# Performance work log

Measured on AMD Instinct MI355X. Metric: run time of the kernel, lower is better.

The kernel has to match this reference:

```python
import jax, jax.numpy as jnp
import numpy as np

N = 50000      # n_nodes
E = 800000     # n_edges
IN_CH = 128
HID = 128
OUT_CH = 64
N_LAYERS = 4


def _linear_params(key, fan_in, fan_out):
    kw, kb = jax.random.split(key)
    bound = 1.0 / np.sqrt(fan_in)
    W = jax.random.uniform(kw, (fan_out, fan_in), jnp.float32, -bound, bound)
    b = jax.random.uniform(kb, (fan_out,), jnp.float32, -bound, bound)
    return W, b


def setup_inputs() -> dict:
    key = jax.random.key(0)
    ks = jax.random.split(key, 5)
    x = jax.random.normal(ks[0], (N, IN_CH), jnp.float32)
    edge_index = jax.random.randint(ks[1], (2, E), 0, N, dtype=jnp.int64)
    W_in, b_in = _linear_params(ks[2], IN_CH, HID)
    conv_keys = jax.random.split(ks[3], N_LAYERS)
    Wc = jnp.stack([_linear_params(k, HID, HID)[0] for k in conv_keys])
    bc = jnp.stack([_linear_params(k, HID, HID)[1] for k in conv_keys])
    W_out, b_out = _linear_params(ks[4], HID * N_LAYERS, OUT_CH)
    return {"x": x, "edge_index": edge_index, "W_in": W_in, "b_in": b_in,
            "Wc": Wc, "bc": bc, "W_out": W_out, "b_out": b_out}


def reference(x, edge_index, W_in, b_in, Wc, bc, W_out, b_out):
    n = x.shape[0]
    # input projection + relu
    x = jax.nn.relu(x @ W_in.T + b_in)
    src, dst = edge_index[0], edge_index[1]
    loop = jnp.arange(n, dtype=edge_index.dtype)
    src_a = jnp.concatenate([src, loop])   # [E+N]
    dst_a = jnp.concatenate([dst, loop])   # [E+N]
    # symmetric-normalized degree (with self loops)
    deg = jax.ops.segment_sum(jnp.ones(src_a.shape[0], x.dtype), dst_a, num_segments=n)
    norm = (deg[src_a] * deg[dst_a]) ** -0.5
    norm = jnp.where(jnp.isinf(norm), 0.0, norm)  # guard deg==0 (original sets inf->0)
    layer_outputs = []
    for i in range(Wc.shape[0]):
        h = x @ Wc[i].T + bc[i]                     # [N, HID]
        msg = h[src_a] * norm[:, None]              # gather + scale  [E+N, HID]
        out = jax.ops.segment_sum(msg, dst_a, num_segments=n)  # scatter-add
        x = jax.nn.relu(out)
        layer_outputs.append(x)
    h = jnp.concatenate(layer_outputs, axis=-1)     # jk_mode='cat' -> [N, HID*L]
    return h @ W_out.T + b_out
```

## Files before the change

kernel.cpp:

```cpp
#include <hip/hip_runtime.h>
#include <hip/hip_bf16.h>

#ifndef MIN
#define MIN(a,b) ((a)<(b)?(a):(b))
#endif

typedef _Float16 half2_t __attribute__((ext_vector_type(2)));
typedef _Float16 half4_t __attribute__((ext_vector_type(4)));
typedef _Float16 half8_t __attribute__((ext_vector_type(8)));
typedef float floatx4 __attribute__((ext_vector_type(4)));

#define BUCKET_SHIFT 6
#define BUCKET_SIZE 64
#define SCHUNK 2048


__global__ void hist_kernel(const int* __restrict__ dst, int E,
                            int* __restrict__ bucketCnt, int NB) {
    __shared__ int h[1024];
    int t = threadIdx.x;
    for (int i = t; i < 1024; i += 256) h[i] = 0;
    __syncthreads();
    for (int e = blockIdx.x * 256 + t; e < E; e += gridDim.x * 256)
        atomicAdd(&h[dst[e] >> BUCKET_SHIFT], 1);
    __syncthreads();
    for (int i = t; i < NB; i += 256)
        if (h[i]) atomicAdd(&bucketCnt[i], h[i]);
}

__global__ void bucket_scan(const int* __restrict__ bucketCnt,
                            int* __restrict__ bucketBase, int* __restrict__ bucketCur,
                            int NB, int E) {
    __shared__ int sm[1024];
    int t = threadIdx.x;
    int v = (t < NB) ? bucketCnt[t] : 0;
    sm[t] = v;
    __syncthreads();
    for (int off = 1; off < 1024; off <<= 1) {
        int add = (t >= off) ? sm[t - off] : 0;
        __syncthreads();
        sm[t] += add;
        __syncthreads();
    }
    if (t < NB) {
        bucketBase[t] = sm[t] - v;
        bucketCur[t] = sm[t] - v;
    }
    if (t == 0) bucketBase[NB] = E;
}

__global__ void scatter_kernel(const int* __restrict__ src, const int* __restrict__ dst,
                               int E, int* __restrict__ bucketCur,
                               unsigned int* __restrict__ rec) {
    __shared__ int hist[1024];
    __shared__ int base[1024];
    int t = threadIdx.x;
    int e0 = blockIdx.x * SCHUNK;
    int e1 = MIN(E, e0 + SCHUNK);
    for (int i = t; i < 1024; i += 256) hist[i] = 0;
    __syncthreads();
    for (int e = e0 + t; e < e1; e += 256)
        atomicAdd(&hist[dst[e] >> BUCKET_SHIFT], 1);
    __syncthreads();
    for (int i = t; i < 1024; i += 256) {
        int c = hist[i];
        base[i] = c ? atomicAdd(&bucketCur[i], c) : 0;
        hist[i] = 0;
    }
    __syncthreads();
    for (int e = e0 + t; e < e1; e += 256) {
        int d = dst[e];
        int b = d >> BUCKET_SHIFT;
        int pos = base[b] + atomicAdd(&hist[b], 1);
        rec[pos] = (unsigned)src[e] | ((unsigned)(d & (BUCKET_SIZE - 1)) << 16);
    }
}

__global__ void bucket_build(const unsigned int* __restrict__ rec,
                             const int* __restrict__ bucketBase,
                             int* __restrict__ rowptr, unsigned short* __restrict__ csr_src,
                             float* __restrict__ dinv, int N, int E) {
    __shared__ int lcnt[256];
    __shared__ int sm[256];
    __shared__ int lcur[64];
    int b = blockIdx.x;
    int t = threadIdx.x;
    int beg = bucketBase[b], end = bucketBase[b + 1];
    lcnt[t] = 0;
    __syncthreads();
    for (int i = beg + t; i < end; i += 256)
        atomicAdd(&lcnt[rec[i] >> 16], 1);
    __syncthreads();
    int v = lcnt[t];
    sm[t] = v;
    __syncthreads();
    for (int off = 1; off < 256; off <<= 1) {
        int add = (t >= off) ? sm[t - off] : 0;
        __syncthreads();
        sm[t] += add;
        __syncthreads();
    }
    int excl = sm[t] - v;
    if (t < BUCKET_SIZE) {
        int node = b * BUCKET_SIZE + t;
        if (node < N) {
            rowptr[node] = beg + excl;
            dinv[node] = rsqrtf((float)(v + 1));
        }
        lcur[t] = beg + excl;
    }
    __syncthreads();
    for (int i = beg + t; i < end; i += 256) {
        unsigned int r = rec[i];
        int pos = atomicAdd(&lcur[r >> 16], 1);
        csr_src[pos] = (unsigned short)(r & 0xFFFFu);
    }
    if (b == 0 && t == 0) rowptr[N] = E;
}


__global__ void cvt_weights(const float* __restrict__ a, _Float16* __restrict__ oa, int na,
                            const float* __restrict__ b, _Float16* __restrict__ ob, int nb,
                            const float* __restrict__ c, _Float16* __restrict__ oc, int nc) {
    int i = blockIdx.x * blockDim.x + threadIdx.x;
    if (i < na) oa[i] = (_Float16)a[i];
    if (i < nb) ob[i] = (_Float16)b[i];
    if (i < nc) oc[i] = (_Float16)c[i];
}


__global__ void agg_kernel(const half2_t* __restrict__ Hb, const float* __restrict__ dinv,
                           const int* __restrict__ rowptr,
                           const unsigned short* __restrict__ csr_src,
                           half2_t* __restrict__ X, int N) {
    int node = blockIdx.x * 4 + (threadIdx.x >> 6);
    int t = threadIdx.x & 63;
    if (node >= N) return;
    float di = dinv[node];
    half2_t hu = Hb[(size_t)node * 64 + t];
    float2 acc;
    acc.x = (float)hu.x * di;
    acc.y = (float)hu.y * di;
    int beg = rowptr[node];
    int end = rowptr[node + 1];

    for (int base = beg; base < end; base += 64) {
        int idx = base + t;
        bool valid = idx < end;
        int s_lane = valid ? (int)csr_src[idx] : node;
        float w_lane = valid ? dinv[s_lane] : 0.0f;
        int m = end - base;
        if (m > 64) m = 64;
        int mm = (m + 7) & ~7;
        for (int j = 0; j < mm; j += 8) {
            int s0 = __shfl(s_lane, j + 0), s1 = __shfl(s_lane, j + 1);
            int s2 = __shfl(s_lane, j + 2), s3 = __shfl(s_lane, j + 3);
            int s4 = __shfl(s_lane, j + 4), s5 = __shfl(s_lane, j + 5);
            int s6 = __shfl(s_lane, j + 6), s7 = __shfl(s_lane, j + 7);
            float w0 = __shfl(w_lane, j + 0), w1 = __shfl(w_lane, j + 1);
            float w2 = __shfl(w_lane, j + 2), w3 = __shfl(w_lane, j + 3);
            float w4 = __shfl(w_lane, j + 4), w5 = __shfl(w_lane, j + 5);
            float w6 = __shfl(w_lane, j + 6), w7 = __shfl(w_lane, j + 7);
            half2_t u0 = Hb[(size_t)s0 * 64 + t];
            half2_t u1 = Hb[(size_t)s1 * 64 + t];
            half2_t u2 = Hb[(size_t)s2 * 64 + t];
            half2_t u3 = Hb[(size_t)s3 * 64 + t];
            half2_t u4 = Hb[(size_t)s4 * 64 + t];
            half2_t u5 = Hb[(size_t)s5 * 64 + t];
            half2_t u6 = Hb[(size_t)s6 * 64 + t];
            half2_t u7 = Hb[(size_t)s7 * 64 + t];
            acc.x = fmaf((float)u0.x, w0, acc.x); acc.y = fmaf((float)u0.y, w0, acc.y);
            acc.x = fmaf((float)u1.x, w1, acc.x); acc.y = fmaf((float)u1.y, w1, acc.y);
            acc.x = fmaf((float)u2.x, w2, acc.x); acc.y = fmaf((float)u2.y, w2, acc.y);
            acc.x = fmaf((float)u3.x, w3, acc.x); acc.y = fmaf((float)u3.y, w3, acc.y);
            acc.x = fmaf((float)u4.x, w4, acc.x); acc.y = fmaf((float)u4.y, w4, acc.y);
            acc.x = fmaf((float)u5.x, w5, acc.x); acc.y = fmaf((float)u5.y, w5, acc.y);
            acc.x = fmaf((float)u6.x, w6, acc.x); acc.y = fmaf((float)u6.y, w6, acc.y);
            acc.x = fmaf((float)u7.x, w7, acc.x); acc.y = fmaf((float)u7.y, w7, acc.y);
        }
    }
    half2_t o;
    o.x = (_Float16)fmaxf(acc.x * di, 0.0f);
    o.y = (_Float16)fmaxf(acc.y * di, 0.0f);
    X[(size_t)node * 256 + t] = o;
}


template <int BN, int KCH, bool A_F16, bool RELU, bool BIAS, bool F16OUT>
__global__ __launch_bounds__(256)
void mfma_gemm(const void* __restrict__ Av, int lda,
               const _Float16* __restrict__ W, int ldw,
               const float* __restrict__ bias,
               void* __restrict__ Cv, int ldc, int M) {
    constexpr int NT = BN / 16;
    __shared__ __align__(16) _Float16 Ws[BN][136];

    int tid = threadIdx.x;
    int rowBase = blockIdx.x * 64;
    int w = tid >> 6;
    int lane = tid & 63;
    int lrow = lane & 15;
    int quad = lane >> 4;
    int kq = quad * 8;
    int gr = rowBase + w * 16 + lrow;

    floatx4 acc[NT];
#pragma unroll
    for (int nt = 0; nt < NT; ++nt) acc[nt] = (floatx4){0.f, 0.f, 0.f, 0.f};

#pragma unroll
    for (int kc = 0; kc < KCH; ++kc) {
#pragma unroll
        for (int i = tid; i < BN * 16; i += 256) {
            int n = i >> 4, k8 = (i & 15) * 8;
            uint4 v = *(const uint4*)(W + (size_t)n * ldw + kc * 128 + k8);
            *(uint4*)(&Ws[n][k8]) = v;
        }
        __syncthreads();

        half8_t a[4];
        if (gr < M) {
            if (A_F16) {
                const _Float16* A = (const _Float16*)Av;
                const _Float16* ap = A + (size_t)gr * lda + kc * 128 + kq;
#pragma unroll
                for (int ks = 0; ks < 4; ++ks)
                    a[ks] = *(const half8_t*)(ap + ks * 32);
            } else {
                const float* A = (const float*)Av;
                const float* ap = A + (size_t)gr * lda + kc * 128 + kq;
#pragma unroll
                for (int ks = 0; ks < 4; ++ks) {
                    float4 v0 = *(const float4*)(ap + ks * 32);
                    float4 v1 = *(const float4*)(ap + ks * 32 + 4);
                    half8_t h;
                    h[0] = (_Float16)v0.x; h[1] = (_Float16)v0.y;
                    h[2] = (_Float16)v0.z; h[3] = (_Float16)v0.w;
                    h[4] = (_Float16)v1.x; h[5] = (_Float16)v1.y;
                    h[6] = (_Float16)v1.z; h[7] = (_Float16)v1.w;
                    a[ks] = h;
                }
            }
        } else {
#pragma unroll
            for (int ks = 0; ks < 4; ++ks)
                a[ks] = (half8_t){0, 0, 0, 0, 0, 0, 0, 0};
        }

#pragma unroll
        for (int ks = 0; ks < 4; ++ks) {
            int kk = ks * 32 + kq;
#pragma unroll
            for (int nt = 0; nt < NT; ++nt) {
                half8_t b = *(const half8_t*)(&Ws[nt * 16 + lrow][kk]);
                acc[nt] = __builtin_amdgcn_mfma_f32_16x16x32_f16(a[ks], b, acc[nt], 0, 0, 0);
            }
        }
        if (kc != KCH - 1) __syncthreads();
    }

#pragma unroll
    for (int nt = 0; nt < NT; ++nt) {
        int col = nt * 16 + lrow;
        float bv = BIAS ? bias[col] : 0.0f;
#pragma unroll
        for (int reg = 0; reg < 4; ++reg) {
            int gr2 = rowBase + w * 16 + quad * 4 + reg;
            if (gr2 < M) {
                float v = acc[nt][reg] + bv;
                if (RELU) v = fmaxf(v, 0.0f);
                if (F16OUT) {
                    _Float16* C = (_Float16*)Cv;
                    C[(size_t)gr2 * ldc + col] = (_Float16)v;
                } else {
                    float* C = (float*)Cv;
                    C[(size_t)gr2 * ldc + col] = v;
                }
            }
        }
    }
}


extern "C" void kernel_launch(void* const* d_in, const int* in_sizes, int n_in,
                              void* d_out, int out_size, void* d_ws, size_t ws_size,
                              hipStream_t stream) {
    const float* x     = (const float*)d_in[0];
    const int*   ei    = (const int*)d_in[1];
    const float* W_in  = (const float*)d_in[2];
    const float* b_in  = (const float*)d_in[3];
    const float* Wc    = (const float*)d_in[4];
    const float* bc    = (const float*)d_in[5];
    const float* W_out = (const float*)d_in[6];
    const float* b_out = (const float*)d_in[7];
    float* out = (float*)d_out;

    const int HID = 128;
    const int N = in_sizes[0] / HID;
    const int E = in_sizes[1] / 2;
    const int L = 4;
    const int* src = ei;
    const int* dst = ei + E;
    const int NB = (N + BUCKET_SIZE - 1) >> BUCKET_SHIFT;

    char* ws = (char*)d_ws;
    size_t off = 0;
    auto carve = [&](size_t bytes) {
        void* p = ws + off;
        off += (bytes + 255) & ~(size_t)255;
        return p;
    };
    float* dinv        = (float*)carve((size_t)N * 4);
    int*   rowptr      = (int*)carve((size_t)(N + 1) * 4);
    unsigned short* csr_src = (unsigned short*)carve((size_t)E * 2);
    unsigned int* rec  = (unsigned int*)carve((size_t)E * 4);
    int*   bucketCnt   = (int*)carve((size_t)1024 * 4);
    int*   bucketBase  = (int*)carve((size_t)1025 * 4);
    int*   bucketCur   = (int*)carve((size_t)1024 * 4);
    _Float16* bufA     = (_Float16*)carve((size_t)N * HID * 2);
    _Float16* bufH     = (_Float16*)carve((size_t)N * HID * 2);
    _Float16* bufXcat  = (_Float16*)carve((size_t)N * 512 * 2);
    _Float16* Wf_in    = (_Float16*)carve((size_t)HID * HID * 2);
    _Float16* Wf_c     = (_Float16*)carve((size_t)L * HID * HID * 2);
    _Float16* Wf_out   = (_Float16*)carve((size_t)64 * 512 * 2);
    (void)ws_size;

    hipMemsetAsync(bucketCnt, 0, (size_t)1024 * 4, stream);
    hist_kernel<<<512, 256, 0, stream>>>(dst, E, bucketCnt, NB);
    bucket_scan<<<1, 1024, 0, stream>>>(bucketCnt, bucketBase, bucketCur, NB, E);
    scatter_kernel<<<(E + SCHUNK - 1) / SCHUNK, 256, 0, stream>>>(src, dst, E, bucketCur, rec);
    bucket_build<<<NB, 256, 0, stream>>>(rec, bucketBase, rowptr, csr_src, dinv, N, E);

    cvt_weights<<<(L * HID * HID + 255) / 256, 256, 0, stream>>>(
        W_in, Wf_in, HID * HID,
        Wc, Wf_c, L * HID * HID,
        W_out, Wf_out, 64 * 512);

    int gemm_blocks = (N + 63) / 64;

    mfma_gemm<128, 1, false, true, true, true>
        <<<gemm_blocks, 256, 0, stream>>>(x, 128, Wf_in, HID, b_in, bufA, HID, N);

    for (int l = 0; l < L; ++l) {
        const void* Ain = (l == 0) ? (const void*)bufA
                                   : (const void*)(bufXcat + (size_t)(l - 1) * 128);
        int lda = (l == 0) ? 128 : 512;
        mfma_gemm<128, 1, true, false, true, true>
            <<<gemm_blocks, 256, 0, stream>>>(Ain, lda, Wf_c + (size_t)l * HID * HID, HID,
                                              bc + (size_t)l * HID, bufH, HID, N);
        agg_kernel<<<(N + 3) / 4, 256, 0, stream>>>((const half2_t*)bufH, dinv, rowptr,
                                                    csr_src,
                                                    (half2_t*)bufXcat + (size_t)l * 64, N);
    }

    mfma_gemm<64, 4, true, false, true, false>
        <<<gemm_blocks, 256, 0, stream>>>(bufXcat, 512, Wf_out, 512, b_out, out, 64, N);
}
```

Before: 326.3 us.

## Prescale GEMM output by dinv, fuse setup kernels, unweighted 16-wide aggregation

The layer GEMM epilogue now multiplies each row by its source-node dinv. The aggregation kernel can then sum neighbour rows without per-edge weight loads or shuffles, and it unrolls 16 gathers per step with padding pointing at a zeroed extra row. The histogram kernel is merged with the weight conversion, and the scatter kernel with the input projection GEMM, into single launches that split work by block index. This cuts per-edge dinv gathers, FMAs and launch count, at the cost of more wasted gathers on padded tails and larger kernels that may hold more registers.

```diff
diff --git a/kernel.cpp b/kernel.cpp
--- a/kernel.cpp
+++ b/kernel.cpp
@@ -15,188 +15,17 @@
 #define SCHUNK 2048
 
 
-__global__ void hist_kernel(const int* __restrict__ dst, int E,
-                            int* __restrict__ bucketCnt, int NB) {
-    __shared__ int h[1024];
-    int t = threadIdx.x;
-    for (int i = t; i < 1024; i += 256) h[i] = 0;
-    __syncthreads();
-    for (int e = blockIdx.x * 256 + t; e < E; e += gridDim.x * 256)
-        atomicAdd(&h[dst[e] >> BUCKET_SHIFT], 1);
-    __syncthreads();
-    for (int i = t; i < NB; i += 256)
-        if (h[i]) atomicAdd(&bucketCnt[i], h[i]);
-}
-
-__global__ void bucket_scan(const int* __restrict__ bucketCnt,
-                            int* __restrict__ bucketBase, int* __restrict__ bucketCur,
-                            int NB, int E) {
-    __shared__ int sm[1024];
-    int t = threadIdx.x;
-    int v = (t < NB) ? bucketCnt[t] : 0;
-    sm[t] = v;
-    __syncthreads();
-    for (int off = 1; off < 1024; off <<= 1) {
-        int add = (t >= off) ? sm[t - off] : 0;
-        __syncthreads();
-        sm[t] += add;
-        __syncthreads();
-    }
-    if (t < NB) {
-        bucketBase[t] = sm[t] - v;
-        bucketCur[t] = sm[t] - v;
-    }
-    if (t == 0) bucketBase[NB] = E;
-}
-
-__global__ void scatter_kernel(const int* __restrict__ src, const int* __restrict__ dst,
-                               int E, int* __restrict__ bucketCur,
-                               unsigned int* __restrict__ rec) {
-    __shared__ int hist[1024];
-    __shared__ int base[1024];
-    int t = threadIdx.x;
-    int e0 = blockIdx.x * SCHUNK;
-    int e1 = MIN(E, e0 + SCHUNK);
-    for (int i = t; i < 1024; i += 256) hist[i] = 0;
-    __syncthreads();
-    for (int e = e0 + t; e < e1; e += 256)
-        atomicAdd(&hist[dst[e] >> BUCKET_SHIFT], 1);
-    __syncthreads();
-    for (int i = t; i < 1024; i += 256) {
-        int c = hist[i];
-        base[i] = c ? atomicAdd(&bucketCur[i], c) : 0;
-        hist[i] = 0;
-    }
-    __syncthreads();
-    for (int e = e0 + t; e < e1; e += 256) {
-        int d = dst[e];
-        int b = d >> BUCKET_SHIFT;
-        int pos = base[b] + atomicAdd(&hist[b], 1);
-        rec[pos] = (unsigned)src[e] | ((unsigned)(d & (BUCKET_SIZE - 1)) << 16);
-    }
-}
-
-__global__ void bucket_build(const unsigned int* __restrict__ rec,
-                             const int* __restrict__ bucketBase,
-                             int* __restrict__ rowptr, unsigned short* __restrict__ csr_src,
-                             float* __restrict__ dinv, int N, int E) {
-    __shared__ int lcnt[256];
-    __shared__ int sm[256];
-    __shared__ int lcur[64];
-    int b = blockIdx.x;
-    int t = threadIdx.x;
-    int beg = bucketBase[b], end = bucketBase[b + 1];
-    lcnt[t] = 0;
-    __syncthreads();
-    for (int i = beg + t; i < end; i += 256)
-        atomicAdd(&lcnt[rec[i] >> 16], 1);
-    __syncthreads();
-    int v = lcnt[t];
-    sm[t] = v;
-    __syncthreads();
-    for (int off = 1; off < 256; off <<= 1) {
-        int add = (t >= off) ? sm[t - off] : 0;
-        __syncthreads();
-        sm[t] += add;
-        __syncthreads();
-    }
-    int excl = sm[t] - v;
-    if (t < BUCKET_SIZE) {
-        int node = b * BUCKET_SIZE + t;
-        if (node < N) {
-            rowptr[node] = beg + excl;
-            dinv[node] = rsqrtf((float)(v + 1));
-        }
-        lcur[t] = beg + excl;
-    }
-    __syncthreads();
-    for (int i = beg + t; i < end; i += 256) {
-        unsigned int r = rec[i];
-        int pos = atomicAdd(&lcur[r >> 16], 1);
-        csr_src[pos] = (unsigned short)(r & 0xFFFFu);
-    }
-    if (b == 0 && t == 0) rowptr[N] = E;
-}
-
-
-__global__ void cvt_weights(const float* __restrict__ a, _Float16* __restrict__ oa, int na,
-                            const float* __restrict__ b, _Float16* __restrict__ ob, int nb,
-                            const float* __restrict__ c, _Float16* __restrict__ oc, int nc) {
-    int i = blockIdx.x * blockDim.x + threadIdx.x;
-    if (i < na) oa[i] = (_Float16)a[i];
-    if (i < nb) ob[i] = (_Float16)b[i];
-    if (i < nc) oc[i] = (_Float16)c[i];
-}
-
-
-__global__ void agg_kernel(const half2_t* __restrict__ Hb, const float* __restrict__ dinv,
-                           const int* __restrict__ rowptr,
-                           const unsigned short* __restrict__ csr_src,
-                           half2_t* __restrict__ X, int N) {
-    int node = blockIdx.x * 4 + (threadIdx.x >> 6);
-    int t = threadIdx.x & 63;
-    if (node >= N) return;
-    float di = dinv[node];
-    half2_t hu = Hb[(size_t)node * 64 + t];
-    float2 acc;
-    acc.x = (float)hu.x * di;
-    acc.y = (float)hu.y * di;
-    int beg = rowptr[node];
-    int end = rowptr[node + 1];
-
-    for (int base = beg; base < end; base += 64) {
-        int idx = base + t;
-        bool valid = idx < end;
-        int s_lane = valid ? (int)csr_src[idx] : node;
-        float w_lane = valid ? dinv[s_lane] : 0.0f;
-        int m = end - base;
-        if (m > 64) m = 64;
-        int mm = (m + 7) & ~7;
-        for (int j = 0; j < mm; j += 8) {
-            int s0 = __shfl(s_lane, j + 0), s1 = __shfl(s_lane, j + 1);
-            int s2 = __shfl(s_lane, j + 2), s3 = __shfl(s_lane, j + 3);
-            int s4 = __shfl(s_lane, j + 4), s5 = __shfl(s_lane, j + 5);
-            int s6 = __shfl(s_lane, j + 6), s7 = __shfl(s_lane, j + 7);
-            float w0 = __shfl(w_lane, j + 0), w1 = __shfl(w_lane, j + 1);
-            float w2 = __shfl(w_lane, j + 2), w3 = __shfl(w_lane, j + 3);
-            float w4 = __shfl(w_lane, j + 4), w5 = __shfl(w_lane, j + 5);
-            float w6 = __shfl(w_lane, j + 6), w7 = __shfl(w_lane, j + 7);
-            half2_t u0 = Hb[(size_t)s0 * 64 + t];
-            half2_t u1 = Hb[(size_t)s1 * 64 + t];
-            half2_t u2 = Hb[(size_t)s2 * 64 + t];
-            half2_t u3 = Hb[(size_t)s3 * 64 + t];
-            half2_t u4 = Hb[(size_t)s4 * 64 + t];
-            half2_t u5 = Hb[(size_t)s5 * 64 + t];
-            half2_t u6 = Hb[(size_t)s6 * 64 + t];
-            half2_t u7 = Hb[(size_t)s7 * 64 + t];
-            acc.x = fmaf((float)u0.x, w0, acc.x); acc.y = fmaf((float)u0.y, w0, acc.y);
-            acc.x = fmaf((float)u1.x, w1, acc.x); acc.y = fmaf((float)u1.y, w1, acc.y);
-            acc.x = fmaf((float)u2.x, w2, acc.x); acc.y = fmaf((float)u2.y, w2, acc.y);
-            acc.x = fmaf((float)u3.x, w3, acc.x); acc.y = fmaf((float)u3.y, w3, acc.y);
-            acc.x = fmaf((float)u4.x, w4, acc.x); acc.y = fmaf((float)u4.y, w4, acc.y);
-            acc.x = fmaf((float)u5.x, w5, acc.x); acc.y = fmaf((float)u5.y, w5, acc.y);
-            acc.x = fmaf((float)u6.x, w6, acc.x); acc.y = fmaf((float)u6.y, w6, acc.y);
-            acc.x = fmaf((float)u7.x, w7, acc.x); acc.y = fmaf((float)u7.y, w7, acc.y);
-        }
-    }
-    half2_t o;
-    o.x = (_Float16)fmaxf(acc.x * di, 0.0f);
-    o.y = (_Float16)fmaxf(acc.y * di, 0.0f);
-    X[(size_t)node * 256 + t] = o;
-}
-
-
-template <int BN, int KCH, bool A_F16, bool RELU, bool BIAS, bool F16OUT>
-__global__ __launch_bounds__(256)
-void mfma_gemm(const void* __restrict__ Av, int lda,
+template <int BN, int KCH, bool A_F16, bool RELU, bool BIAS, bool SCALE, bool F16OUT>
+__device__ __forceinline__
+void gemm_body(int bid, const void* __restrict__ Av, int lda,
                const _Float16* __restrict__ W, int ldw,
-               const float* __restrict__ bias,
+               const float* __restrict__ bias, const float* __restrict__ dinv,
                void* __restrict__ Cv, int ldc, int M) {
     constexpr int NT = BN / 16;
     __shared__ __align__(16) _Float16 Ws[BN][136];
 
     int tid = threadIdx.x;
-    int rowBase = blockIdx.x * 64;
+    int rowBase = bid * 64;
     int w = tid >> 6;
     int lane = tid & 63;
     int lrow = lane & 15;
@@ -269,6 +98,7 @@
             if (gr2 < M) {
                 float v = acc[nt][reg] + bv;
                 if (RELU) v = fmaxf(v, 0.0f);
+                if (SCALE) v *= dinv[gr2];
                 if (F16OUT) {
                     _Float16* C = (_Float16*)Cv;
                     C[(size_t)gr2 * ldc + col] = (_Float16)v;
@@ -279,6 +109,183 @@
             }
         }
     }
+}
+
+template <int BN, int KCH, bool A_F16, bool RELU, bool BIAS, bool SCALE, bool F16OUT>
+__global__ __launch_bounds__(256)
+void mfma_gemm(const void* __restrict__ Av, int lda,
+               const _Float16* __restrict__ W, int ldw,
+               const float* __restrict__ bias, const float* __restrict__ dinv,
+               void* __restrict__ Cv, int ldc, int M) {
+    gemm_body<BN, KCH, A_F16, RELU, BIAS, SCALE, F16OUT>(
+        blockIdx.x, Av, lda, W, ldw, bias, dinv, Cv, ldc, M);
+}
+
+
+__global__ __launch_bounds__(256)
+void k_hist_cvt(const int* __restrict__ dst, int E, int* __restrict__ bucketCnt, int NB,
+                const float* __restrict__ a, _Float16* __restrict__ oa, int na,
+                const float* __restrict__ b, _Float16* __restrict__ ob, int nb,
+                const float* __restrict__ c, _Float16* __restrict__ oc, int nc,
+                _Float16* __restrict__ zrow) {
+    __shared__ int h[1024];
+    int t = threadIdx.x;
+    if (blockIdx.x < 512) {
+        for (int i = t; i < 1024; i += 256) h[i] = 0;
+        __syncthreads();
+        for (int e = blockIdx.x * 256 + t; e < E; e += 512 * 256)
+            atomicAdd(&h[dst[e] >> BUCKET_SHIFT], 1);
+        __syncthreads();
+        for (int i = t; i < NB; i += 256)
+            if (h[i]) atomicAdd(&bucketCnt[i], h[i]);
+    } else {
+        int i = (blockIdx.x - 512) * 256 + t;
+        if (i < na) oa[i] = (_Float16)a[i];
+        if (i < nb) ob[i] = (_Float16)b[i];
+        if (i < nc) oc[i] = (_Float16)c[i];
+        if (i < 128) zrow[i] = (_Float16)0.0f;
+    }
+}
+
+__global__ void bucket_scan(const int* __restrict__ bucketCnt,
+                            int* __restrict__ bucketBase, int* __restrict__ bucketCur,
+                            int NB, int E) {
+    __shared__ int sm[1024];
+    int t = threadIdx.x;
+    int v = (t < NB) ? bucketCnt[t] : 0;
+    sm[t] = v;
+    __syncthreads();
+    for (int off = 1; off < 1024; off <<= 1) {
+        int add = (t >= off) ? sm[t - off] : 0;
+        __syncthreads();
+        sm[t] += add;
+        __syncthreads();
+    }
+    if (t < NB) {
+        bucketBase[t] = sm[t] - v;
+        bucketCur[t] = sm[t] - v;
+    }
+    if (t == 0) bucketBase[NB] = E;
+}
+
+
+__global__ __launch_bounds__(256)
+void k_scatter_proj(const int* __restrict__ src, const int* __restrict__ dst, int E,
+                    int* __restrict__ bucketCur, unsigned int* __restrict__ rec, int SB,
+                    const float* __restrict__ A, const _Float16* __restrict__ W,
+                    const float* __restrict__ bias, _Float16* __restrict__ Cout, int M) {
+    __shared__ int hist[1024];
+    __shared__ int base[1024];
+    if (blockIdx.x < SB) {
+        int t = threadIdx.x;
+        int e0 = blockIdx.x * SCHUNK;
+        int e1 = MIN(E, e0 + SCHUNK);
+        for (int i = t; i < 1024; i += 256) hist[i] = 0;
+        __syncthreads();
+        for (int e = e0 + t; e < e1; e += 256)
+            atomicAdd(&hist[dst[e] >> BUCKET_SHIFT], 1);
+        __syncthreads();
+        for (int i = t; i < 1024; i += 256) {
+            int c = hist[i];
+            base[i] = c ? atomicAdd(&bucketCur[i], c) : 0;
+            hist[i] = 0;
+        }
+        __syncthreads();
+        for (int e = e0 + t; e < e1; e += 256) {
+            int d = dst[e];
+            int bk = d >> BUCKET_SHIFT;
+            int pos = base[bk] + atomicAdd(&hist[bk], 1);
+            rec[pos] = (unsigned)src[e] | ((unsigned)(d & (BUCKET_SIZE - 1)) << 16);
+        }
+    } else {
+        gemm_body<128, 1, false, true, true, false, true>(
+            blockIdx.x - SB, A, 128, W, 128, bias, nullptr, Cout, 128, M);
+    }
+}
+
+__global__ void bucket_build(const unsigned int* __restrict__ rec,
+                             const int* __restrict__ bucketBase,
+                             int* __restrict__ rowptr, unsigned short* __restrict__ csr_src,
+                             float* __restrict__ dinv, int N, int E) {
+    __shared__ int lcnt[256];
+    __shared__ int sm[256];
+    __shared__ int lcur[64];
+    int b = blockIdx.x;
+    int t = threadIdx.x;
+    int beg = bucketBase[b], end = bucketBase[b + 1];
+    lcnt[t] = 0;
+    __syncthreads();
+    for (int i = beg + t; i < end; i += 256)
+        atomicAdd(&lcnt[rec[i] >> 16], 1);
+    __syncthreads();
+    int v = lcnt[t];
+    sm[t] = v;
+    __syncthreads();
+    for (int off = 1; off < 256; off <<= 1) {
+        int add = (t >= off) ? sm[t - off] : 0;
+        __syncthreads();
+        sm[t] += add;
+        __syncthreads();
+    }
+    int excl = sm[t] - v;
+    if (t < BUCKET_SIZE) {
+        int node = b * BUCKET_SIZE + t;
+        if (node < N) {
+            rowptr[node] = beg + excl;
+            dinv[node] = rsqrtf((float)(v + 1));
+        }
+        lcur[t] = beg + excl;
+    }
+    __syncthreads();
+    for (int i = beg + t; i < end; i += 256) {
+        unsigned int r = rec[i];
+        int pos = atomicAdd(&lcur[r >> 16], 1);
+        csr_src[pos] = (unsigned short)(r & 0xFFFFu);
+    }
+    if (b == 0 && t == 0) rowptr[N] = E;
+}
+
+
+__global__ __launch_bounds__(256)
+void agg_kernel(const half2_t* __restrict__ Hb, const float* __restrict__ dinv,
+                const int* __restrict__ rowptr,
+                const unsigned short* __restrict__ csr_src,
+                half2_t* __restrict__ X, int N) {
+    int node = blockIdx.x * 4 + (threadIdx.x >> 6);
+    int t = threadIdx.x & 63;
+    if (node >= N) return;
+    float di = dinv[node];
+    half2_t hu = Hb[(size_t)node * 64 + t];
+    float2 acc;
+    acc.x = (float)hu.x;
+    acc.y = (float)hu.y;
+    int beg = rowptr[node];
+    int end = rowptr[node + 1];
+
+    for (int base = beg; base < end; base += 64) {
+        int idx = base + t;
+        int s_lane = (idx < end) ? (int)csr_src[idx] : N;
+        int m = end - base;
+        if (m > 64) m = 64;
+        int mm = (m + 15) & ~15;
+        for (int j = 0; j < mm; j += 16) {
+            int s[16];
+#pragma unroll
+            for (int k = 0; k < 16; ++k) s[k] = __shfl(s_lane, j + k);
+            half2_t u[16];
+#pragma unroll
+            for (int k = 0; k < 16; ++k) u[k] = Hb[(size_t)s[k] * 64 + t];
+#pragma unroll
+            for (int k = 0; k < 16; ++k) {
+                acc.x += (float)u[k].x;
+                acc.y += (float)u[k].y;
+            }
+        }
+    }
+    half2_t o;
+    o.x = (_Float16)fmaxf(acc.x * di, 0.0f);
+    o.y = (_Float16)fmaxf(acc.y * di, 0.0f);
+    X[(size_t)node * 256 + t] = o;
 }
 
 
@@ -318,41 +325,42 @@
     int*   bucketBase  = (int*)carve((size_t)1025 * 4);
     int*   bucketCur   = (int*)carve((size_t)1024 * 4);
     _Float16* bufA     = (_Float16*)carve((size_t)N * HID * 2);
-    _Float16* bufH     = (_Float16*)carve((size_t)N * HID * 2);
+    _Float16* bufH     = (_Float16*)carve((size_t)(N + 1) * HID * 2);
     _Float16* bufXcat  = (_Float16*)carve((size_t)N * 512 * 2);
     _Float16* Wf_in    = (_Float16*)carve((size_t)HID * HID * 2);
     _Float16* Wf_c     = (_Float16*)carve((size_t)L * HID * HID * 2);
     _Float16* Wf_out   = (_Float16*)carve((size_t)64 * 512 * 2);
     (void)ws_size;
 
+    int gemm_blocks = (N + 63) / 64;
+    int SB = (E + SCHUNK - 1) / SCHUNK;
+
     hipMemsetAsync(bucketCnt, 0, (size_t)1024 * 4, stream);
-    hist_kernel<<<512, 256, 0, stream>>>(dst, E, bucketCnt, NB);
-    bucket_scan<<<1, 1024, 0, stream>>>(bucketCnt, bucketBase, bucketCur, NB, E);
-    scatter_kernel<<<(E + SCHUNK - 1) / SCHUNK, 256, 0, stream>>>(src, dst, E, bucketCur, rec);
-    bucket_build<<<NB, 256, 0, stream>>>(rec, bucketBase, rowptr, csr_src, dinv, N, E);
-
-    cvt_weights<<<(L * HID * HID + 255) / 256, 256, 0, stream>>>(
+    k_hist_cvt<<<512 + 256, 256, 0, stream>>>(
+        dst, E, bucketCnt, NB,
         W_in, Wf_in, HID * HID,
         Wc, Wf_c, L * HID * HID,
-        W_out, Wf_out, 64 * 512);
-
-    int gemm_blocks = (N + 63) / 64;
-
-    mfma_gemm<128, 1, false, true, true, true>
-        <<<gemm_blocks, 256, 0, stream>>>(x, 128, Wf_in, HID, b_in, bufA, HID, N);
+        W_out, Wf_out, 64 * 512,
+        bufH + (size_t)N * HID);
+    bucket_scan<<<1, 1024, 0, stream>>>(bucketCnt, bucketBase, bucketCur, NB, E);
+    k_scatter_proj<<<SB + gemm_blocks, 256, 0, stream>>>(
+        src, dst, E, bucketCur, rec, SB,
+        x, Wf_in, b_in, bufA, N);
+    bucket_build<<<NB, 256, 0, stream>>>(rec, bucketBase, rowptr, csr_src, dinv, N, E);
 
     for (int l = 0; l < L; ++l) {
         const void* Ain = (l == 0) ? (const void*)bufA
                                    : (const void*)(bufXcat + (size_t)(l - 1) * 128);
         int lda = (l == 0) ? 128 : 512;
-        mfma_gemm<128, 1, true, false, true, true>
+        mfma_gemm<128, 1, true, false, true, true, true>
             <<<gemm_blocks, 256, 0, stream>>>(Ain, lda, Wf_c + (size_t)l * HID * HID, HID,
-                                              bc + (size_t)l * HID, bufH, HID, N);
+                                              bc + (size_t)l * HID, dinv, bufH, HID, N);
         agg_kernel<<<(N + 3) / 4, 256, 0, stream>>>((const half2_t*)bufH, dinv, rowptr,
                                                     csr_src,
                                                     (half2_t*)bufXcat + (size_t)l * 64, N);
     }
 
-    mfma_gemm<64, 4, true, false, true, false>
-        <<<gemm_blocks, 256, 0, stream>>>(bufXcat, 512, Wf_out, 512, b_out, out, 64, N);
-}
+    mfma_gemm<64, 4, true, false, true, false, false>
+        <<<gemm_blocks, 256, 0, stream>>>(bufXcat, 512, Wf_out, 512, b_out, nullptr,
+                                          out, 64, N);
+}
```

Measured after the change: 320.7 us. About the same (-1.7%).
